# Kernel optimization log

Hardware: AMD Instinct MI355X
Metric: run time of the kernel (lower is better)

The kernel has to match this reference:

```python
import jax, jax.numpy as jnp
import numpy as np
import math

IN_C = 512
OUT_C = 512
K = 3
STYLE = 512
EPS = 1e-8
MOD_SCALE = 1.0 / math.sqrt(STYLE)        # EqualLinear scale (lr_mul=1)
CONV_SCALE = 1.0 / math.sqrt(IN_C * K * K)  # ModulatedConv2d scale


def setup_inputs() -> dict:
    key = jax.random.key(0)
    k1, k2, k3, k4 = jax.random.split(key, 4)
    return {
        "x": jax.random.normal(k1, (8, IN_C, 64, 64), dtype=jnp.float32),
        "style": jax.random.normal(k2, (8, STYLE), dtype=jnp.float32),
        "mod_weight": jax.random.normal(k3, (IN_C, STYLE), dtype=jnp.float32),
        "mod_bias": jnp.ones((IN_C,), dtype=jnp.float32),
        "weight": jax.random.normal(k4, (1, OUT_C, IN_C, K, K), dtype=jnp.float32),
    }


def _per_sample_conv(xi, wi):
    # xi: [in_c, H, W], wi: [out_c, in_c, K, K]
    out = jax.lax.conv_general_dilated(
        xi[None], wi, window_strides=(1, 1), padding="SAME",
        dimension_numbers=("NCHW", "OIHW", "NCHW"))
    return out[0]


def reference(x, style, mod_weight, mod_bias, weight):
    # EqualLinear modulation: s = style @ (W*scale)^T + bias  -> [B, in_c]
    s = style @ (mod_weight * MOD_SCALE).T + mod_bias
    # per-sample modulated weight: [B, out_c, in_c, K, K]
    w = CONV_SCALE * weight * s[:, None, :, None, None]
    demod = jax.lax.rsqrt(jnp.sum(w * w, axis=(2, 3, 4), keepdims=True) + EPS)
    w = w * demod
    # grouped conv (groups=batch) == vmap of per-sample conv
    out = jax.vmap(_per_sample_conv)(x, w)  # [B, out_c, H, W]
    return out
```

## Files before the change

### kernel.cpp

```cpp
#include <hip/hip_runtime.h>
#include <hip/hip_bf16.h>

typedef __attribute__((ext_vector_type(8))) short bf16x8;
typedef __attribute__((ext_vector_type(16))) float f32x16;
typedef unsigned int u32;

#define MOD_SCALE 0.04419417382415922f
#define CONV_SCALE 0.014731391274719742f

__device__ __forceinline__ unsigned short f2bf(float f) {
  union { float f; u32 u; } v; v.f = f;
  u32 r = v.u + 0x7fffu + ((v.u >> 16) & 1u);
  return (unsigned short)(r >> 16);
}

__device__ __forceinline__ void gload_lds16(const void* g, void* l) {
  __builtin_amdgcn_global_load_lds(
      (const __attribute__((address_space(1))) u32*)g,
      (__attribute__((address_space(3))) u32*)l, 16, 0, 0);
}

__global__ void k_prep(const float* __restrict__ wsrc, ushort* __restrict__ wb,
                       float* __restrict__ wsq, float* __restrict__ zerobuf,
                       const float* __restrict__ style, const float* __restrict__ mw,
                       const float* __restrict__ mb, float* __restrict__ s) {
  if (blockIdx.x < 1024) {
    int idx = blockIdx.x * 256 + threadIdx.x;
    int oc = idx >> 9, ic = idx & 511;
    int icb = ic >> 4, icr = ic & 15;
    if (blockIdx.x == 0 && threadIdx.x < 16) zerobuf[threadIdx.x] = 0.f;
    const float* wp = wsrc + (size_t)idx * 9;
    float sq = 0.f;
    #pragma unroll
    for (int tap = 0; tap < 9; ++tap) {
      float v = wp[tap];
      sq += v * v;
      wb[((tap * 32 + icb) * 512 + oc) * 16 + icr] = f2bf(v);
    }
    wsq[idx] = sq;
  } else {
    int idx = (blockIdx.x - 1024) * 256 + threadIdx.x;
    int b = idx >> 9, ic = idx & 511;
    const float4* wr = (const float4*)(mw + ic * 512);
    const float4* sr = (const float4*)(style + b * 512);
    float acc = 0.f;
    #pragma unroll 4
    for (int k = 0; k < 128; ++k) {
      float4 a = wr[k], c = sr[k];
      acc += a.x * c.x + a.y * c.y + a.z * c.z + a.w * c.w;
    }
    s[idx] = acc * MOD_SCALE + mb[ic];
  }
}

__global__ void k_demod(const float* __restrict__ wsq, const float* __restrict__ s,
                        float* __restrict__ dscale) {
  int idx = blockIdx.x * 256 + threadIdx.x;
  int b = idx >> 9, oc = idx & 511;
  const float4* wq = (const float4*)(wsq + oc * 512);
  const float4* sp = (const float4*)(s + b * 512);
  float acc = 0.f;
  #pragma unroll 4
  for (int k = 0; k < 128; ++k) {
    float4 a = wq[k], c = sp[k];
    acc += a.x * c.x * c.x + a.y * c.y * c.y + a.z * c.z * c.z + a.w * c.w * c.w;
  }
  dscale[idx] = CONV_SCALE * rsqrtf(CONV_SCALE * CONV_SCALE * acc + 1e-8f);
}

__global__ void k_xform(const float* __restrict__ x, const float* __restrict__ s,
                        ushort* __restrict__ xsb) {
  const int y = blockIdx.x, b = blockIdx.y;
  const int t = threadIdx.x;
  const int px = t & 63, icq = t >> 6;
  #pragma unroll
  for (int i = 0; i < 8; ++i) {
    int icb = i * 4 + icq;
    union { ushort u[16]; uint4 v[2]; } pk;
    #pragma unroll
    for (int j = 0; j < 16; ++j) {
      int ic = icb * 16 + j;
      float v = x[(b * 512 + ic) * 4096 + y * 64 + px] * s[b * 512 + ic];
      pk.u[j] = f2bf(v);
    }
    ushort* dst = xsb + ((size_t)((b * 64 + y) * 32 + icb) * 64 + px) * 16;
    *(uint4*)dst = pk.v[0];
    *(uint4*)(dst + 8) = pk.v[1];
  }
}

#define ABYTES 18432
#define BBYTES 21120
#define BUFB   39552
__global__ __launch_bounds__(256, 2) void k_conv(
    const ushort* __restrict__ wb, const ushort* __restrict__ xsb,
    const float* __restrict__ dscale, const float* __restrict__ zerobuf,
    float* __restrict__ out) {
  const int yb = blockIdx.x, ocb = blockIdx.y, b = blockIdx.z;
  const int t = threadIdx.x;
  const int wv = t >> 6, l = t & 63;
  const int lc = l & 31, lh = l >> 5;
  const int y0 = yb * 8, oc0 = ocb * 64;

  extern __shared__ char smem[];
  float* dss = (float*)(smem + 2 * BUFB);
  if (t < 64) dss[t] = dscale[b * 512 + oc0 + t];

  f32x16 acc[2][2][2];
  #pragma unroll
  for (int rr = 0; rr < 2; ++rr)
    #pragma unroll
    for (int ocf = 0; ocf < 2; ++ocf)
      #pragma unroll
      for (int pxf = 0; pxf < 2; ++pxf)
        #pragma unroll
        for (int k = 0; k < 16; ++k)
          acc[rr][ocf][pxf][k] = 0.f;

  const char* asrc[5];
  #pragma unroll
  for (int i = 0; i < 5; ++i) {
    int cid = i * 256 + t;
    int tap = cid >> 7, rem = cid & 127;
    int oc_l = rem >> 1, h = rem & 1;
    asrc[i] = (const char*)wb + (size_t)tap * 524288 + (oc0 + oc_l) * 32 + h * 16;
  }
  const char* bsrc[6];
  int bstride[6];
  #pragma unroll
  for (int i = 0; i < 6; ++i) {
    int cid = i * 256 + t;
    int r = cid / 132, rem = cid - r * 132;
    int yy = y0 - 1 + r;
    bool interior = (rem >= 2) && (rem < 130) && ((unsigned)yy < 64u);
    bsrc[i] = interior
        ? (const char*)xsb + (size_t)(b * 64 + yy) * 65536 + (rem - 2) * 16
        : (const char*)zerobuf;
    bstride[i] = interior ? 2048 : 0;
  }

  auto STAGE = [&](int bo, int icb) {
    char* Ab = smem + bo;
    char* Bb = Ab + ABYTES;
    const int aoff = icb * 16384;
    #pragma unroll
    for (int i = 0; i < 4; ++i)
      gload_lds16(asrc[i] + aoff, Ab + i * 4096 + wv * 1024);
    if (t < 128)
      gload_lds16(asrc[4] + aoff, Ab + 16384 + wv * 1024);
    #pragma unroll
    for (int i = 0; i < 5; ++i)
      gload_lds16(bsrc[i] + icb * bstride[i], Bb + i * 4096 + wv * 1024);
    if (t < 40)
      gload_lds16(bsrc[5] + icb * bstride[5], Bb + 20480);
  };

  auto COMPUTE = [&](int bo) {
    const char* Ab = smem + bo;
    const char* Bb = Ab + ABYTES;
    const int arow = lc * 32 + lh * 16;
    #pragma unroll
    for (int dx = 0; dx < 3; ++dx) {
      bf16x8 bfr[4][2];
      #pragma unroll
      for (int j = 0; j < 4; ++j)
        #pragma unroll
        for (int pxf = 0; pxf < 2; ++pxf)
          bfr[j][pxf] = *(const bf16x8*)(Bb + (wv * 2 + j) * 2112 + (pxf * 32 + dx + lc) * 32 + lh * 16);
      #pragma unroll
      for (int dy = 0; dy < 3; ++dy) {
        const int tap = dy * 3 + dx;
        bf16x8 af[2];
        #pragma unroll
        for (int ocf = 0; ocf < 2; ++ocf)
          af[ocf] = *(const bf16x8*)(Ab + tap * 2048 + ocf * 1024 + arow);
        #pragma unroll
        for (int rr = 0; rr < 2; ++rr)
          #pragma unroll
          for (int ocf = 0; ocf < 2; ++ocf)
            #pragma unroll
            for (int pxf = 0; pxf < 2; ++pxf)
              acc[rr][ocf][pxf] = __builtin_amdgcn_mfma_f32_32x32x16_bf16(
                  af[ocf], bfr[rr + dy][pxf], acc[rr][ocf][pxf], 0, 0, 0);
      }
    }
  };

  STAGE(0, 0);
  __syncthreads();
  #pragma unroll 1
  for (int it = 0; it < 32; ++it) {
    if (it < 31) STAGE(((it + 1) & 1) * BUFB, it + 1);
    COMPUTE((it & 1) * BUFB);
    __syncthreads();
  }

  #pragma unroll
  for (int rr = 0; rr < 2; ++rr) {
    const int y_row = y0 + wv * 2 + rr;
    #pragma unroll
    for (int ocf = 0; ocf < 2; ++ocf) {
      #pragma unroll
      for (int pxf = 0; pxf < 2; ++pxf) {
        #pragma unroll
        for (int reg = 0; reg < 16; ++reg) {
          int oc_l = ocf * 32 + (reg & 3) + 8 * (reg >> 2) + 4 * lh;
          out[(size_t)(b * 512 + oc0 + oc_l) * 4096 + y_row * 64 + pxf * 32 + lc]
              = acc[rr][ocf][pxf][reg] * dss[oc_l];
        }
      }
    }
  }
}

extern "C" void kernel_launch(void* const* d_in, const int* in_sizes, int n_in,
                              void* d_out, int out_size, void* d_ws, size_t ws_size,
                              hipStream_t stream) {
  const float* x     = (const float*)d_in[0];
  const float* style = (const float*)d_in[1];
  const float* mw    = (const float*)d_in[2];
  const float* mb    = (const float*)d_in[3];
  const float* wsrc  = (const float*)d_in[4];
  float* out = (float*)d_out;

  char* ws = (char*)d_ws;
  float*  zerobuf = (float*)(ws + 0);
  float*  s       = (float*)(ws + 256);
  float*  dscale  = (float*)(ws + 16640);
  float*  wsq     = (float*)(ws + 33024);
  ushort* wb      = (ushort*)(ws + 1081600);
  ushort* xsb     = (ushort*)(ws + 5800192);

  hipFuncSetAttribute(reinterpret_cast<const void*>(k_conv),
                      hipFuncAttributeMaxDynamicSharedMemorySize, 2 * BUFB + 256);

  k_prep<<<dim3(1040), dim3(256), 0, stream>>>(wsrc, wb, wsq, zerobuf, style, mw, mb, s);
  k_demod<<<dim3(16), dim3(256), 0, stream>>>(wsq, s, dscale);
  k_xform<<<dim3(64, 8), dim3(256), 0, stream>>>(x, s, xsb);
  k_conv<<<dim3(8, 8, 8), dim3(256), 2 * BUFB + 256, stream>>>(wb, xsb, dscale, zerobuf, out);
}
```

Baseline: 185.6 us.

## Swizzle LDS tiles, fuse demod into conv kernel, unroll double-buffer loop

```diff
diff --git a/kernel.cpp b/kernel.cpp
--- a/kernel.cpp
+++ b/kernel.cpp
@@ -19,6 +19,8 @@
       (const __attribute__((address_space(1))) u32*)g,
       (__attribute__((address_space(3))) u32*)l, 16, 0, 0);
 }
+
+__device__ __forceinline__ int swz(int c) { return c ^ ((c >> 3) & 1); }
 
 __global__ void k_prep(const float* __restrict__ wsrc, ushort* __restrict__ wb,
                        float* __restrict__ wsq, float* __restrict__ zerobuf,
@@ -53,21 +55,6 @@
   }
 }
 
-__global__ void k_demod(const float* __restrict__ wsq, const float* __restrict__ s,
-                        float* __restrict__ dscale) {
-  int idx = blockIdx.x * 256 + threadIdx.x;
-  int b = idx >> 9, oc = idx & 511;
-  const float4* wq = (const float4*)(wsq + oc * 512);
-  const float4* sp = (const float4*)(s + b * 512);
-  float acc = 0.f;
-  #pragma unroll 4
-  for (int k = 0; k < 128; ++k) {
-    float4 a = wq[k], c = sp[k];
-    acc += a.x * c.x * c.x + a.y * c.y * c.y + a.z * c.z * c.z + a.w * c.w * c.w;
-  }
-  dscale[idx] = CONV_SCALE * rsqrtf(CONV_SCALE * CONV_SCALE * acc + 1e-8f);
-}
-
 __global__ void k_xform(const float* __restrict__ x, const float* __restrict__ s,
                         ushort* __restrict__ xsb) {
   const int y = blockIdx.x, b = blockIdx.y;
@@ -94,8 +81,8 @@
 #define BUFB   39552
 __global__ __launch_bounds__(256, 2) void k_conv(
     const ushort* __restrict__ wb, const ushort* __restrict__ xsb,
-    const float* __restrict__ dscale, const float* __restrict__ zerobuf,
-    float* __restrict__ out) {
+    const float* __restrict__ wsq, const float* __restrict__ s,
+    const float* __restrict__ zerobuf, float* __restrict__ out) {
   const int yb = blockIdx.x, ocb = blockIdx.y, b = blockIdx.z;
   const int t = threadIdx.x;
   const int wv = t >> 6, l = t & 63;
@@ -103,8 +90,8 @@
   const int y0 = yb * 8, oc0 = ocb * 64;
 
   extern __shared__ char smem[];
-  float* dss = (float*)(smem + 2 * BUFB);
-  if (t < 64) dss[t] = dscale[b * 512 + oc0 + t];
+  float* red = (float*)(smem + 2 * BUFB);
+  float* dss = (float*)(smem + 2 * BUFB + 1024);
 
   f32x16 acc[2][2][2];
   #pragma unroll
@@ -121,8 +108,9 @@
   #pragma unroll
   for (int i = 0; i < 5; ++i) {
     int cid = i * 256 + t;
-    int tap = cid >> 7, rem = cid & 127;
-    int oc_l = rem >> 1, h = rem & 1;
+    int tap = cid >> 7, pc = cid & 127;
+    int c = swz(pc);
+    int oc_l = c >> 1, h = c & 1;
     asrc[i] = (const char*)wb + (size_t)tap * 524288 + (oc0 + oc_l) * 32 + h * 16;
   }
   const char* bsrc[6];
@@ -130,14 +118,25 @@
   #pragma unroll
   for (int i = 0; i < 6; ++i) {
     int cid = i * 256 + t;
-    int r = cid / 132, rem = cid - r * 132;
-    int yy = y0 - 1 + r;
-    bool interior = (rem >= 2) && (rem < 130) && ((unsigned)yy < 64u);
+    int pr = cid / 132, prem = cid - pr * 132;
+    int lrem = swz(prem);
+    int yy = y0 - 1 + pr;
+    bool interior = (lrem >= 2) && (lrem < 130) && ((unsigned)yy < 64u);
     bsrc[i] = interior
-        ? (const char*)xsb + (size_t)(b * 64 + yy) * 65536 + (rem - 2) * 16
+        ? (const char*)xsb + (size_t)(b * 64 + yy) * 65536 + (lrem - 2) * 16
         : (const char*)zerobuf;
     bstride[i] = interior ? 2048 : 0;
   }
+
+  int aswzo; { int c = lc * 2 + lh; aswzo = swz(c) * 16; }
+  int bswzo[3][2];
+  #pragma unroll
+  for (int dx = 0; dx < 3; ++dx)
+    #pragma unroll
+    for (int pxf = 0; pxf < 2; ++pxf) {
+      int c = (pxf * 32 + dx + lc) * 2 + lh;
+      bswzo[dx][pxf] = swz(c) * 16;
+    }
 
   auto STAGE = [&](int bo, int icb) {
     char* Ab = smem + bo;
@@ -158,7 +157,6 @@
   auto COMPUTE = [&](int bo) {
     const char* Ab = smem + bo;
     const char* Bb = Ab + ABYTES;
-    const int arow = lc * 32 + lh * 16;
     #pragma unroll
     for (int dx = 0; dx < 3; ++dx) {
       bf16x8 bfr[4][2];
@@ -166,14 +164,14 @@
       for (int j = 0; j < 4; ++j)
         #pragma unroll
         for (int pxf = 0; pxf < 2; ++pxf)
-          bfr[j][pxf] = *(const bf16x8*)(Bb + (wv * 2 + j) * 2112 + (pxf * 32 + dx + lc) * 32 + lh * 16);
+          bfr[j][pxf] = *(const bf16x8*)(Bb + (wv * 2 + j) * 2112 + bswzo[dx][pxf]);
       #pragma unroll
       for (int dy = 0; dy < 3; ++dy) {
         const int tap = dy * 3 + dx;
         bf16x8 af[2];
         #pragma unroll
         for (int ocf = 0; ocf < 2; ++ocf)
-          af[ocf] = *(const bf16x8*)(Ab + tap * 2048 + ocf * 1024 + arow);
+          af[ocf] = *(const bf16x8*)(Ab + tap * 2048 + ocf * 1024 + aswzo);
         #pragma unroll
         for (int rr = 0; rr < 2; ++rr)
           #pragma unroll
@@ -187,11 +185,31 @@
   };
 
   STAGE(0, 0);
+
+  {
+    const int oc_l = t & 63, kq = t >> 6;
+    const float4* wq = (const float4*)(wsq + (oc0 + oc_l) * 512) + kq * 32;
+    const float4* sp = (const float4*)(s + b * 512) + kq * 32;
+    float part = 0.f;
+    #pragma unroll 4
+    for (int k = 0; k < 32; ++k) {
+      float4 a = wq[k], c = sp[k];
+      part += a.x * c.x * c.x + a.y * c.y * c.y + a.z * c.z * c.z + a.w * c.w * c.w;
+    }
+    red[t] = part;
+  }
   __syncthreads();
+  if (t < 64)
+    dss[t] = CONV_SCALE * rsqrtf(
+        CONV_SCALE * CONV_SCALE * (red[t] + red[t + 64] + red[t + 128] + red[t + 192]) + 1e-8f);
+
   #pragma unroll 1
-  for (int it = 0; it < 32; ++it) {
-    if (it < 31) STAGE(((it + 1) & 1) * BUFB, it + 1);
-    COMPUTE((it & 1) * BUFB);
+  for (int it = 0; it < 32; it += 2) {
+    STAGE(BUFB, it + 1);
+    COMPUTE(0);
+    __syncthreads();
+    if (it < 30) STAGE(0, it + 2);
+    COMPUTE(BUFB);
     __syncthreads();
   }
 
@@ -226,16 +244,14 @@
   char* ws = (char*)d_ws;
   float*  zerobuf = (float*)(ws + 0);
   float*  s       = (float*)(ws + 256);
-  float*  dscale  = (float*)(ws + 16640);
   float*  wsq     = (float*)(ws + 33024);
   ushort* wb      = (ushort*)(ws + 1081600);
   ushort* xsb     = (ushort*)(ws + 5800192);
 
   hipFuncSetAttribute(reinterpret_cast<const void*>(k_conv),
-                      hipFuncAttributeMaxDynamicSharedMemorySize, 2 * BUFB + 256);
+                      hipFuncAttributeMaxDynamicSharedMemorySize, 2 * BUFB + 1280);
 
   k_prep<<<dim3(1040), dim3(256), 0, stream>>>(wsrc, wb, wsq, zerobuf, style, mw, mb, s);
-  k_demod<<<dim3(16), dim3(256), 0, stream>>>(wsq, s, dscale);
   k_xform<<<dim3(64, 8), dim3(256), 0, stream>>>(x, s, xsb);
-  k_conv<<<dim3(8, 8, 8), dim3(256), 2 * BUFB + 256, stream>>>(wb, xsb, dscale, zerobuf, out);
-}
+  k_conv<<<dim3(8, 8, 8), dim3(256), 2 * BUFB + 1280, stream>>>(wb, xsb, wsq, s, zerobuf, out);
+}
```

After: 172.7 us. 1.07x faster.

## Fuse prep kernels, compute demod directly, and retile conv waves for B-fragment reuse

Applied to the files above, without the earlier changes.

```diff
diff --git a/kernel.cpp b/kernel.cpp
--- a/kernel.cpp
+++ b/kernel.cpp
@@ -20,78 +20,103 @@
       (__attribute__((address_space(3))) u32*)l, 16, 0, 0);
 }
 
-__global__ void k_prep(const float* __restrict__ wsrc, ushort* __restrict__ wb,
-                       float* __restrict__ wsq, float* __restrict__ zerobuf,
-                       const float* __restrict__ style, const float* __restrict__ mw,
-                       const float* __restrict__ mb, float* __restrict__ s) {
-  if (blockIdx.x < 1024) {
-    int idx = blockIdx.x * 256 + threadIdx.x;
-    int oc = idx >> 9, ic = idx & 511;
-    int icb = ic >> 4, icr = ic & 15;
-    if (blockIdx.x == 0 && threadIdx.x < 16) zerobuf[threadIdx.x] = 0.f;
-    const float* wp = wsrc + (size_t)idx * 9;
-    float sq = 0.f;
-    #pragma unroll
-    for (int tap = 0; tap < 9; ++tap) {
-      float v = wp[tap];
-      sq += v * v;
-      wb[((tap * 32 + icb) * 512 + oc) * 16 + icr] = f2bf(v);
-    }
-    wsq[idx] = sq;
-  } else {
-    int idx = (blockIdx.x - 1024) * 256 + threadIdx.x;
-    int b = idx >> 9, ic = idx & 511;
-    const float4* wr = (const float4*)(mw + ic * 512);
-    const float4* sr = (const float4*)(style + b * 512);
-    float acc = 0.f;
-    #pragma unroll 4
-    for (int k = 0; k < 128; ++k) {
-      float4 a = wr[k], c = sr[k];
-      acc += a.x * c.x + a.y * c.y + a.z * c.z + a.w * c.w;
-    }
-    s[idx] = acc * MOD_SCALE + mb[ic];
-  }
-}
-
-__global__ void k_demod(const float* __restrict__ wsq, const float* __restrict__ s,
-                        float* __restrict__ dscale) {
+__global__ void k_style(const float* __restrict__ style, const float* __restrict__ mw,
+                        const float* __restrict__ mb, float* __restrict__ s) {
   int idx = blockIdx.x * 256 + threadIdx.x;
-  int b = idx >> 9, oc = idx & 511;
-  const float4* wq = (const float4*)(wsq + oc * 512);
-  const float4* sp = (const float4*)(s + b * 512);
+  int b = idx >> 9, ic = idx & 511;
+  const float4* wr = (const float4*)(mw + ic * 512);
+  const float4* sr = (const float4*)(style + b * 512);
   float acc = 0.f;
   #pragma unroll 4
   for (int k = 0; k < 128; ++k) {
-    float4 a = wq[k], c = sp[k];
-    acc += a.x * c.x * c.x + a.y * c.y * c.y + a.z * c.z * c.z + a.w * c.w * c.w;
-  }
-  dscale[idx] = CONV_SCALE * rsqrtf(CONV_SCALE * CONV_SCALE * acc + 1e-8f);
-}
-
-__global__ void k_xform(const float* __restrict__ x, const float* __restrict__ s,
-                        ushort* __restrict__ xsb) {
-  const int y = blockIdx.x, b = blockIdx.y;
+    float4 a = wr[k], c = sr[k];
+    acc += a.x * c.x + a.y * c.y + a.z * c.z + a.w * c.w;
+  }
+  s[idx] = acc * MOD_SCALE + mb[ic];
+}
+
+__global__ void k_pre(const float* __restrict__ wsrc, ushort* __restrict__ wb,
+                      float* __restrict__ zerobuf, const float* __restrict__ x,
+                      const float* __restrict__ s, ushort* __restrict__ xsb,
+                      float* __restrict__ dscale) {
+  __shared__ float wtile[2304];
   const int t = threadIdx.x;
-  const int px = t & 63, icq = t >> 6;
-  #pragma unroll
-  for (int i = 0; i < 8; ++i) {
-    int icb = i * 4 + icq;
-    union { ushort u[16]; uint4 v[2]; } pk;
-    #pragma unroll
-    for (int j = 0; j < 16; ++j) {
-      int ic = icb * 16 + j;
-      float v = x[(b * 512 + ic) * 4096 + y * 64 + px] * s[b * 512 + ic];
-      pk.u[j] = f2bf(v);
-    }
-    ushort* dst = xsb + ((size_t)((b * 64 + y) * 32 + icb) * 64 + px) * 16;
-    *(uint4*)dst = pk.v[0];
-    *(uint4*)(dst + 8) = pk.v[1];
+  if (blockIdx.x < 1024) {
+    const float4* s4 = (const float4*)(wsrc + (size_t)blockIdx.x * 2304);
+    float4* w4 = (float4*)wtile;
+    w4[t] = s4[t];
+    w4[t + 256] = s4[t + 256];
+    if (t < 64) w4[t + 512] = s4[t + 512];
+    __syncthreads();
+    int idx = blockIdx.x * 256 + t;
+    int oc = idx >> 9, ic = idx & 511;
+    int icb = ic >> 4, icr = ic & 15;
+    if (blockIdx.x == 0 && t < 16) zerobuf[t] = 0.f;
+    #pragma unroll
+    for (int tap = 0; tap < 9; ++tap)
+      wb[((tap * 32 + icb) * 512 + oc) * 16 + icr] = f2bf(wtile[t * 9 + tap]);
+  } else if (blockIdx.x < 1536) {
+    int bid2 = blockIdx.x - 1024;
+    const int y = bid2 & 63, b = bid2 >> 6;
+    const int px = t & 63, icq = t >> 6;
+    #pragma unroll
+    for (int i = 0; i < 8; ++i) {
+      int icb = i * 4 + icq;
+      union { ushort u[16]; uint4 v[2]; } pk;
+      #pragma unroll
+      for (int j = 0; j < 16; ++j) {
+        int ic = icb * 16 + j;
+        float v = x[(b * 512 + ic) * 4096 + y * 64 + px] * s[b * 512 + ic];
+        pk.u[j] = f2bf(v);
+      }
+      ushort* dst = xsb + ((size_t)((b * 64 + y) * 32 + icb) * 64 + px) * 16;
+      *(uint4*)dst = pk.v[0];
+      *(uint4*)(dst + 8) = pk.v[1];
+    }
+  } else {
+    int bid3 = blockIdx.x - 1536;
+    int b = bid3 >> 2, og = bid3 & 3;
+    float* ssq = wtile;
+    float* part = wtile + 512;
+    {
+      float v0 = s[b * 512 + t], v1 = s[b * 512 + t + 256];
+      ssq[t] = v0 * v0;
+      ssq[t + 256] = v1 * v1;
+    }
+    __syncthreads();
+    const int oc = og * 128 + (t >> 1), ih = t & 1;
+    const float4* wp = (const float4*)(wsrc + (size_t)oc * 4608 + ih * 2304);
+    float acc = 0.f;
+    #pragma unroll 2
+    for (int si = 0; si < 64; ++si) {
+      const int ic0 = ih * 256 + si * 4;
+      float4 f0 = wp[si * 9 + 0], f1 = wp[si * 9 + 1], f2 = wp[si * 9 + 2];
+      float4 f3 = wp[si * 9 + 3], f4v = wp[si * 9 + 4], f5 = wp[si * 9 + 5];
+      float4 f6 = wp[si * 9 + 6], f7 = wp[si * 9 + 7], f8 = wp[si * 9 + 8];
+      float g0 = ssq[ic0], g1 = ssq[ic0 + 1], g2 = ssq[ic0 + 2], g3 = ssq[ic0 + 3];
+      float s0 = f0.x*f0.x + f0.y*f0.y + f0.z*f0.z + f0.w*f0.w
+               + f1.x*f1.x + f1.y*f1.y + f1.z*f1.z + f1.w*f1.w + f2.x*f2.x;
+      float s1 = f2.y*f2.y + f2.z*f2.z + f2.w*f2.w
+               + f3.x*f3.x + f3.y*f3.y + f3.z*f3.z + f3.w*f3.w + f4v.x*f4v.x + f4v.y*f4v.y;
+      float s2 = f4v.z*f4v.z + f4v.w*f4v.w + f5.x*f5.x + f5.y*f5.y + f5.z*f5.z + f5.w*f5.w
+               + f6.x*f6.x + f6.y*f6.y + f6.z*f6.z;
+      float s3 = f6.w*f6.w + f7.x*f7.x + f7.y*f7.y + f7.z*f7.z + f7.w*f7.w
+               + f8.x*f8.x + f8.y*f8.y + f8.z*f8.z + f8.w*f8.w;
+      acc += s0 * g0 + s1 * g1 + s2 * g2 + s3 * g3;
+    }
+    part[t] = acc;
+    __syncthreads();
+    if (t < 128) {
+      float tot = part[2 * t] + part[2 * t + 1];
+      dscale[b * 512 + og * 128 + t] = CONV_SCALE * rsqrtf(CONV_SCALE * CONV_SCALE * tot + 1e-8f);
+    }
   }
 }
 
 #define ABYTES 18432
 #define BBYTES 21120
 #define BUFB   39552
+#define SMEMSZ (2 * BUFB + 256)
 __global__ __launch_bounds__(256, 2) void k_conv(
     const ushort* __restrict__ wb, const ushort* __restrict__ xsb,
     const float* __restrict__ dscale, const float* __restrict__ zerobuf,
@@ -100,30 +125,29 @@
   const int t = threadIdx.x;
   const int wv = t >> 6, l = t & 63;
   const int lc = l & 31, lh = l >> 5;
+  const int wvr = wv >> 1, wvp = wv & 1;
   const int y0 = yb * 8, oc0 = ocb * 64;
 
   extern __shared__ char smem[];
   float* dss = (float*)(smem + 2 * BUFB);
   if (t < 64) dss[t] = dscale[b * 512 + oc0 + t];
 
-  f32x16 acc[2][2][2];
-  #pragma unroll
-  for (int rr = 0; rr < 2; ++rr)
+  f32x16 acc[4][2];
+  #pragma unroll
+  for (int rr = 0; rr < 4; ++rr)
     #pragma unroll
     for (int ocf = 0; ocf < 2; ++ocf)
       #pragma unroll
-      for (int pxf = 0; pxf < 2; ++pxf)
-        #pragma unroll
-        for (int k = 0; k < 16; ++k)
-          acc[rr][ocf][pxf][k] = 0.f;
+      for (int k = 0; k < 16; ++k)
+        acc[rr][ocf][k] = 0.f;
 
   const char* asrc[5];
   #pragma unroll
   for (int i = 0; i < 5; ++i) {
     int cid = i * 256 + t;
-    int tap = cid >> 7, rem = cid & 127;
-    int oc_l = rem >> 1, h = rem & 1;
-    asrc[i] = (const char*)wb + (size_t)tap * 524288 + (oc0 + oc_l) * 32 + h * 16;
+    int tap = cid >> 7, cc = cid & 127;
+    int oc_l = cc >> 1, h = cc & 1;
+    asrc[i] = (const char*)wb + (size_t)tap * 524288 + (size_t)(oc0 + oc_l) * 32 + h * 16;
   }
   const char* bsrc[6];
   int bstride[6];
@@ -139,6 +163,9 @@
     bstride[i] = interior ? 2048 : 0;
   }
 
+  const int apo = (lc * 2 + lh) * 16;
+  const int bco = (wvp * 32 + lc) * 32 + lh * 16;
+
   auto STAGE = [&](int bo, int icb) {
     char* Ab = smem + bo;
     char* Bb = Ab + ABYTES;
@@ -157,57 +184,52 @@
 
   auto COMPUTE = [&](int bo) {
     const char* Ab = smem + bo;
-    const char* Bb = Ab + ABYTES;
-    const int arow = lc * 32 + lh * 16;
+    const char* Bb = smem + bo + ABYTES;
     #pragma unroll
     for (int dx = 0; dx < 3; ++dx) {
-      bf16x8 bfr[4][2];
-      #pragma unroll
-      for (int j = 0; j < 4; ++j)
-        #pragma unroll
-        for (int pxf = 0; pxf < 2; ++pxf)
-          bfr[j][pxf] = *(const bf16x8*)(Bb + (wv * 2 + j) * 2112 + (pxf * 32 + dx + lc) * 32 + lh * 16);
-      #pragma unroll
-      for (int dy = 0; dy < 3; ++dy) {
-        const int tap = dy * 3 + dx;
-        bf16x8 af[2];
+      bf16x8 bfr[6];
+      #pragma unroll
+      for (int j = 0; j < 6; ++j)
+        bfr[j] = *(const bf16x8*)(Bb + (wvr * 4 + j) * 2112 + dx * 32 + bco);
+      bf16x8 af[3][2];
+      #pragma unroll
+      for (int dy = 0; dy < 3; ++dy)
         #pragma unroll
         for (int ocf = 0; ocf < 2; ++ocf)
-          af[ocf] = *(const bf16x8*)(Ab + tap * 2048 + ocf * 1024 + arow);
+          af[dy][ocf] = *(const bf16x8*)(Ab + (dy * 3 + dx) * 2048 + ocf * 1024 + apo);
+      #pragma unroll
+      for (int dy = 0; dy < 3; ++dy)
         #pragma unroll
-        for (int rr = 0; rr < 2; ++rr)
+        for (int rr = 0; rr < 4; ++rr)
           #pragma unroll
           for (int ocf = 0; ocf < 2; ++ocf)
-            #pragma unroll
-            for (int pxf = 0; pxf < 2; ++pxf)
-              acc[rr][ocf][pxf] = __builtin_amdgcn_mfma_f32_32x32x16_bf16(
-                  af[ocf], bfr[rr + dy][pxf], acc[rr][ocf][pxf], 0, 0, 0);
-      }
+            acc[rr][ocf] = __builtin_amdgcn_mfma_f32_32x32x16_bf16(
+                af[dy][ocf], bfr[rr + dy], acc[rr][ocf], 0, 0, 0);
     }
   };
 
   STAGE(0, 0);
   __syncthreads();
   #pragma unroll 1
-  for (int it = 0; it < 32; ++it) {
-    if (it < 31) STAGE(((it + 1) & 1) * BUFB, it + 1);
-    COMPUTE((it & 1) * BUFB);
-    __syncthreads();
-  }
-
-  #pragma unroll
-  for (int rr = 0; rr < 2; ++rr) {
-    const int y_row = y0 + wv * 2 + rr;
+  for (int it = 0; it < 32; it += 2) {
+    STAGE(BUFB, it + 1);
+    COMPUTE(0);
+    __syncthreads();
+    if (it < 30) STAGE(0, it + 2);
+    COMPUTE(BUFB);
+    __syncthreads();
+  }
+
+  #pragma unroll
+  for (int rr = 0; rr < 4; ++rr) {
+    const int y_row = y0 + wvr * 4 + rr;
     #pragma unroll
     for (int ocf = 0; ocf < 2; ++ocf) {
       #pragma unroll
-      for (int pxf = 0; pxf < 2; ++pxf) {
-        #pragma unroll
-        for (int reg = 0; reg < 16; ++reg) {
-          int oc_l = ocf * 32 + (reg & 3) + 8 * (reg >> 2) + 4 * lh;
-          out[(size_t)(b * 512 + oc0 + oc_l) * 4096 + y_row * 64 + pxf * 32 + lc]
-              = acc[rr][ocf][pxf][reg] * dss[oc_l];
-        }
+      for (int reg = 0; reg < 16; ++reg) {
+        int oc_l = ocf * 32 + (reg & 3) + 8 * (reg >> 2) + 4 * lh;
+        out[(size_t)(b * 512 + oc0 + oc_l) * 4096 + y_row * 64 + wvp * 32 + lc]
+            = acc[rr][ocf][reg] * dss[oc_l];
       }
     }
   }
@@ -227,15 +249,13 @@
   float*  zerobuf = (float*)(ws + 0);
   float*  s       = (float*)(ws + 256);
   float*  dscale  = (float*)(ws + 16640);
-  float*  wsq     = (float*)(ws + 33024);
   ushort* wb      = (ushort*)(ws + 1081600);
   ushort* xsb     = (ushort*)(ws + 5800192);
 
   hipFuncSetAttribute(reinterpret_cast<const void*>(k_conv),
-                      hipFuncAttributeMaxDynamicSharedMemorySize, 2 * BUFB + 256);
-
-  k_prep<<<dim3(1040), dim3(256), 0, stream>>>(wsrc, wb, wsq, zerobuf, style, mw, mb, s);
-  k_demod<<<dim3(16), dim3(256), 0, stream>>>(wsq, s, dscale);
-  k_xform<<<dim3(64, 8), dim3(256), 0, stream>>>(x, s, xsb);
-  k_conv<<<dim3(8, 8, 8), dim3(256), 2 * BUFB + 256, stream>>>(wb, xsb, dscale, zerobuf, out);
-}
+                      hipFuncAttributeMaxDynamicSharedMemorySize, SMEMSZ);
+
+  k_style<<<dim3(16), dim3(256), 0, stream>>>(style, mw, mb, s);
+  k_pre<<<dim3(1568), dim3(256), 0, stream>>>(wsrc, wb, zerobuf, x, s, xsb, dscale);
+  k_conv<<<dim3(8, 8, 8), dim3(256), SMEMSZ, stream>>>(wb, xsb, dscale, zerobuf, out);
+}
```

New measurement: 232.8 us. +25.4%, slower.
